# Performance work log

Hardware: AMD Instinct MI355X
Metric: run time of the kernel (lower is better)

## Reference

```python
import jax, jax.numpy as jnp
import numpy as np
from jax import lax

SLOPE = 0.1  # LeakyRelu(0.1)
DN = ('NCHW', 'OIHW', 'NCHW')


def _xavier(key, shape, cin, cout):
    bound = 2.0 / (cout + cin) ** 0.5
    return jax.random.uniform(key, shape, jnp.float32, -bound, bound)


def setup_inputs() -> dict:
    key = jax.random.key(0)
    ks = jax.random.split(key, 9)
    x = jax.random.normal(ks[0], (8, 3, 256, 256), jnp.float32)
    # Conv2d always adds bias in forward (even with bias=False flag), so biases included.
    w1 = _xavier(ks[1], (48, 3, 3, 3), 3, 48)
    b1 = _xavier(ks[2], (48,), 3, 48)
    w2 = _xavier(ks[3], (48, 48, 3, 3), 48, 48)
    b2 = _xavier(ks[4], (48,), 48, 48)
    w3 = _xavier(ks[5], (48, 48, 3, 3), 48, 48)
    b3 = _xavier(ks[6], (48,), 48, 48)
    w4 = _xavier(ks[7], (48, 48, 3, 3), 48, 48)
    b4 = _xavier(ks[8], (48,), 48, 48)
    return {"x": x, "w1": w1, "b1": b1, "w2": w2, "b2": b2,
            "w3": w3, "b3": b3, "w4": w4, "b4": b4}


def _convblock(x, w, b):
    # 3x3 stride-1 pad-1 conv (original does unfold + matmul; math identical)
    y = lax.conv_general_dilated(x, w, (1, 1), [(1, 1), (1, 1)], dimension_numbers=DN)
    y = y + b[None, :, None, None]
    # LeakyReLU: x * (mask*(1-s)+s) == where(x>0, x, s*x)
    return jnp.where(y > 0, y, SLOPE * y)


def _maxpool2(x):
    n, c, h, w = x.shape
    return x.reshape(n, c, h // 2, 2, w // 2, 2).max(axis=(3, 5))


def reference(x, w1, b1, w2, b2, w3, b3, w4, b4):
    # encoder01: conv(3->48) + conv(48->48) + maxpool
    h = _convblock(x, w1, b1)
    h = _convblock(h, w2, b2)
    h = _maxpool2(h)
    # encoder2: conv(48->48) + maxpool
    h = _convblock(h, w3, b3)
    h = _maxpool2(h)
    # encoder3: conv(48->48) + maxpool
    h = _convblock(h, w4, b4)
    h = _maxpool2(h)
    return h  # (8, 48, 32, 32)
```

## Files before the change

### kernel.cpp

```cpp
#include <hip/hip_runtime.h>
#include <hip/hip_bf16.h>

typedef _Float16 half_t;
typedef _Float16 f16x8 __attribute__((ext_vector_type(8)));
typedef _Float16 f16x4 __attribute__((ext_vector_type(4)));
typedef float f32x4 __attribute__((ext_vector_type(4)));

#define LEAKY 0.1f

__global__ __launch_bounds__(512) void prep_w_k(const float* __restrict__ w1,
                                                const float* __restrict__ w2,
                                                half_t* __restrict__ wp1,
                                                half_t* __restrict__ wp2)
{
    int t = blockIdx.x * 512 + threadIdx.x;
    if (t < 1920) {
        int co = t / 40, kk = t % 40;
        float v = 0.f;
        if (kk < 27) {
            int tap = kk / 3, ci = kk % 3;
            v = w1[((co * 3 + ci) * 3 + tap / 3) * 3 + tap % 3];
        }
        wp1[t] = (half_t)v;
        return;
    }
    int t2 = t - 1920;
    if (t2 >= 23040) return;
    int tap = t2 / 2304, r = t2 % 2304;
    int ci8 = r / 384, r2 = r % 384;
    int mm = r2 / 24, r3 = r2 % 24;
    int nt = r3 / 8, j = r3 % 8;
    int co = nt * 16 + mm, ci = ci8 * 8 + j;
    float v = 0.f;
    if (tap < 9) v = w2[((co * 48 + ci) * 3 + tap / 3) * 3 + tap % 3];
    wp2[t2] = (half_t)v;
}

__global__ __launch_bounds__(512, 4) void conv12_k(const float* __restrict__ x,
                                                   const half_t* __restrict__ wp1,
                                                   const float* __restrict__ b1,
                                                   const half_t* __restrict__ wp2,
                                                   const float* __restrict__ b2,
                                                   const float* __restrict__ w3,
                                                   const float* __restrict__ w4,
                                                   half_t* __restrict__ wp34,
                                                   half_t* __restrict__ out)
{
    __shared__ alignas(16) half_t in_t[624 * 56];
    __shared__ alignas(16) half_t xt[21][36][4];
    __shared__ alignas(16) half_t w1t[1920];

    const int tid = threadIdx.x;
    const int n = blockIdx.z;
    const int hblk = blockIdx.x * 16, wblk = blockIdx.y * 32;
    const int lane = tid & 63, hp = tid >> 6;
    const int m = lane & 15, g = lane >> 4;

    {
        int bid = blockIdx.x + 16 * (blockIdx.y + 8 * blockIdx.z);
        int t2 = bid * 512 + tid;
        if (t2 < 46080) {
            int layer = t2 / 23040, r0 = t2 % 23040;
            int tap = r0 / 2304, r = r0 % 2304;
            int ci8 = r / 384, r2 = r % 384;
            int mm = r2 / 24, r3 = r2 % 24;
            int nt = r3 / 8, j = r3 % 8;
            int co = nt * 16 + mm, ci = ci8 * 8 + j;
            const float* src = layer ? w4 : w3;
            float v = 0.f;
            if (tap < 9) v = src[((co * 48 + ci) * 3 + tap / 3) * 3 + tap % 3];
            wp34[t2] = (half_t)v;
        }
    }
    {
        const uint4* s = (const uint4*)wp1;
        uint4* d = (uint4*)w1t;
        if (tid < 240) d[tid] = s[tid];
    }
    for (int c = tid; c < 2268; c += 512) {
        int ci = c / 756, rem = c % 756;
        int row = rem / 36, col = rem % 36;
        int gh = hblk - 2 + row, gw = wblk - 2 + col;
        float v = 0.f;
        if ((unsigned)gh < 256u && (unsigned)gw < 256u)
            v = x[((n * 3 + ci) * 256 + gh) * 256 + gw];
        xt[row][col][ci] = (half_t)v;
    }
    __syncthreads();

    int xoff[8];
    #pragma unroll
    for (int j = 0; j < 8; ++j) {
        int k = g * 8 + j;
        int tap = k / 3, ci = k - 3 * tap;
        int dr = tap / 3, ds = tap - 3 * dr;
        xoff[j] = (k < 27) ? ((dr * 36 + ds) * 8 + ci * 2) : 0;
    }
    f16x8 wf[3];
    float bb1[12];
    #pragma unroll
    for (int nt = 0; nt < 3; ++nt) {
        wf[nt] = *(const f16x8*)((const char*)w1t + (nt * 16 + m) * 80 + g * 16);
        float4 bv = *(const float4*)(b1 + nt * 16 + 4 * g);
        bb1[nt * 4 + 0] = bv.x; bb1[nt * 4 + 1] = bv.y;
        bb1[nt * 4 + 2] = bv.z; bb1[nt * 4 + 3] = bv.w;
    }
    const char* xtb = (const char*)&xt[0][0][0];
    for (int t = hp; t < 39; t += 8) {
        int px = t * 16 + m;
        int row = px / 34, col = px - row * 34;
        int pxb = (row * 36 + col) * 8;
        f16x8 pf;
        #pragma unroll
        for (int j = 0; j < 8; ++j)
            pf[j] = *(const half_t*)(xtb + pxb + xoff[j]);
        bool inb = ((unsigned)(hblk - 1 + row) < 256u) && ((unsigned)(wblk - 1 + col) < 256u);
        #pragma unroll
        for (int nt = 0; nt < 3; ++nt) {
            f32x4 d = {0.f, 0.f, 0.f, 0.f};
            d = __builtin_amdgcn_mfma_f32_16x16x32_f16(wf[nt], pf, d, 0, 0, 0);
            f16x4 o;
            #pragma unroll
            for (int j = 0; j < 4; ++j) {
                float v = d[j] + bb1[nt * 4 + j];
                v = v > 0.f ? v : LEAKY * v;
                o[j] = inb ? (half_t)v : (half_t)0.f;
            }
            *(f16x4*)(&in_t[px * 56 + nt * 16 + 4 * g]) = o;
        }
    }

    const int hpar = m & 1, wloc = m >> 1;
    const int abase = hp * 7616;
    const char* ib = (const char*)in_t;
    const char* bp = (const char*)wp2 + m * 48;

    f16x8 bf[4][3], af[4];

#define BLOAD(S) { \
    int kc = 4 * (S) + g; int tap = kc / 6, ci8 = kc - tap * 6; \
    int boff = tap * 4608 + ci8 * 768; \
    bf[(S) & 3][0] = *(const f16x8*)(bp + boff); \
    bf[(S) & 3][1] = *(const f16x8*)(bp + boff + 16); \
    bf[(S) & 3][2] = *(const f16x8*)(bp + boff + 32); }
#define ALOAD(S) { \
    int kc = 4 * (S) + g; int tap = kc / 6, ci8 = kc - tap * 6; \
    int dr = tap / 3, ds = tap - 3 * dr; \
    if (tap == 9) { dr = 0; ds = 0; } \
    int aoff = ((hpar + dr) * 34 + (wloc + ds)) * 112 + ci8 * 16 + abase; \
    af[0] = *(const f16x8*)(ib + aoff); \
    af[1] = *(const f16x8*)(ib + aoff + 896); \
    af[2] = *(const f16x8*)(ib + aoff + 1792); \
    af[3] = *(const f16x8*)(ib + aoff + 2688); }
#define MM(P) { \
    __builtin_amdgcn_s_setprio(1); \
    _Pragma("unroll") \
    for (int mt = 0; mt < 4; ++mt) { \
        acc[mt][0] = __builtin_amdgcn_mfma_f32_16x16x32_f16(af[mt], bf[P][0], acc[mt][0], 0, 0, 0); \
        acc[mt][1] = __builtin_amdgcn_mfma_f32_16x16x32_f16(af[mt], bf[P][1], acc[mt][1], 0, 0, 0); \
        acc[mt][2] = __builtin_amdgcn_mfma_f32_16x16x32_f16(af[mt], bf[P][2], acc[mt][2], 0, 0, 0); \
    } \
    __builtin_amdgcn_s_setprio(0); }

    BLOAD(0); BLOAD(1); BLOAD(2); BLOAD(3);
    __syncthreads();

    f32x4 acc[4][3];
    #pragma unroll
    for (int mt = 0; mt < 4; ++mt)
        #pragma unroll
        for (int nt = 0; nt < 3; ++nt)
            acc[mt][nt] = (f32x4){0.f, 0.f, 0.f, 0.f};

    #pragma unroll
    for (int s = 0; s < 14; ++s) {
        ALOAD(s);
        MM(s & 3);
        if (s < 10) BLOAD(s + 4);
    }
#undef BLOAD
#undef ALOAD
#undef MM

    int hq = blockIdx.x * 8 + hp;
    #pragma unroll
    for (int nt = 0; nt < 3; ++nt) {
        int co = nt * 16 + m;
        float bb = b2[co];
        #pragma unroll
        for (int mt = 0; mt < 4; ++mt) {
            float pmax = -1e30f;
            #pragma unroll
            for (int j = 0; j < 4; ++j) {
                float v = acc[mt][nt][j] + bb;
                v = v > 0.f ? v : LEAKY * v;
                pmax = fmaxf(pmax, v);
            }
            int wq = blockIdx.y * 16 + mt * 4 + g;
            out[((n * 128 + hq) * 128 + wq) * 48 + co] = (half_t)pmax;
        }
    }
}

template<int H, int W, int MT, int NTS, bool FINAL>
__global__ __launch_bounds__(256, 4)
void convpool4_k(const half_t* __restrict__ in,
                 const half_t* __restrict__ wp,
                 const float* __restrict__ bias,
                 void* __restrict__ outv)
{
    constexpr int HO = H / 2, WO = W / 2;
    constexpr int TC = 8 * MT + 2;
    constexpr int NU4 = 10 * TC * 6;

    __shared__ alignas(16) half_t in_t[10][TC][56];

    int tid = threadIdx.x;
    int n = blockIdx.z & 7, ntb = blockIdx.z >> 3;
    int hblk = blockIdx.x * 8, wblk = blockIdx.y * (8 * MT);
    int lane = tid & 63, hp = tid >> 6;
    int m = lane & 15, g = lane >> 4;
    int hpar = m & 1, wloc = m >> 1;

    {
        const uint4* s4 = (const uint4*)in;
        uint4* d = (uint4*)&in_t[0][0][0];
        #pragma unroll
        for (int i = 0; i < (NU4 + 255) / 256; ++i) {
            int c = tid + i * 256;
            if (c < NU4) {
                int row = c / (TC * 6);
                int rem = c - row * (TC * 6);
                int pix = rem / 6;
                int sub = rem - pix * 6;
                int gh = hblk - 1 + row, gw = wblk - 1 + pix;
                uint4 v = {0u, 0u, 0u, 0u};
                if ((unsigned)gh < (unsigned)H && (unsigned)gw < (unsigned)W)
                    v = s4[((n * H + gh) * W + gw) * 6 + sub];
                d[(row * TC + pix) * 7 + sub] = v;
            }
        }
    }

    int abase = hp * 2 * TC * 112;
    const char* ib = (const char*)&in_t[0][0][0];
    const char* bp = (const char*)wp + m * 48 + ntb * NTS * 16;

    f16x8 bf[4][NTS], a[MT];

#define BLOAD(S) { \
    int kc = 4 * (S) + g; int tap = kc / 6, ci8 = kc - tap * 6; \
    int boff = tap * 4608 + ci8 * 768; \
    _Pragma("unroll") \
    for (int nt = 0; nt < NTS; ++nt) \
        bf[(S) & 3][nt] = *(const f16x8*)(bp + boff + nt * 16); }

    BLOAD(0); BLOAD(1); BLOAD(2); BLOAD(3);

    f32x4 acc[MT][NTS];
    #pragma unroll
    for (int mt = 0; mt < MT; ++mt)
        #pragma unroll
        for (int nt = 0; nt < NTS; ++nt)
            acc[mt][nt] = (f32x4){0.f, 0.f, 0.f, 0.f};

    __syncthreads();

    #pragma unroll
    for (int s = 0; s < 14; ++s) {
        int kc = 4 * s + g;
        int tap = kc / 6, ci8 = kc - tap * 6;
        int dr = tap / 3, ds = tap - 3 * dr;
        if (tap == 9) { dr = 0; ds = 0; }
        int aoff = ((hpar + dr) * TC + (wloc + ds)) * 112 + ci8 * 16;
        #pragma unroll
        for (int mt = 0; mt < MT; ++mt)
            a[mt] = *(const f16x8*)(ib + abase + aoff + mt * 896);
        __builtin_amdgcn_s_setprio(1);
        #pragma unroll
        for (int mt = 0; mt < MT; ++mt)
            #pragma unroll
            for (int nt = 0; nt < NTS; ++nt)
                acc[mt][nt] = __builtin_amdgcn_mfma_f32_16x16x32_f16(a[mt], bf[s & 3][nt], acc[mt][nt], 0, 0, 0);
        __builtin_amdgcn_s_setprio(0);
        if (s < 10) BLOAD(s + 4);
    }
#undef BLOAD

    int hq = blockIdx.x * 4 + hp;
    #pragma unroll
    for (int nt = 0; nt < NTS; ++nt) {
        int co = (ntb * NTS + nt) * 16 + m;
        float bb = bias[co];
        #pragma unroll
        for (int mt = 0; mt < MT; ++mt) {
            float pmax = -1e30f;
            #pragma unroll
            for (int j = 0; j < 4; ++j) {
                float v = acc[mt][nt][j] + bb;
                v = v > 0.f ? v : LEAKY * v;
                pmax = fmaxf(pmax, v);
            }
            int wq = blockIdx.y * (4 * MT) + mt * 4 + g;
            if (FINAL)
                ((float*)outv)[(((long)n * 48 + co) * HO + hq) * WO + wq] = pmax;
            else
                ((half_t*)outv)[((n * HO + hq) * WO + wq) * 48 + co] = (half_t)pmax;
        }
    }
}

extern "C" void kernel_launch(void* const* d_in, const int* in_sizes, int n_in,
                              void* d_out, int out_size, void* d_ws, size_t ws_size,
                              hipStream_t stream)
{
    const float* x  = (const float*)d_in[0];
    const float* w1 = (const float*)d_in[1];
    const float* b1 = (const float*)d_in[2];
    const float* w2 = (const float*)d_in[3];
    const float* b2 = (const float*)d_in[4];
    const float* w3 = (const float*)d_in[5];
    const float* b3 = (const float*)d_in[6];
    const float* w4 = (const float*)d_in[7];
    const float* b4 = (const float*)d_in[8];

    half_t* Wb = (half_t*)d_ws;
    half_t* wp1  = Wb;
    half_t* wp2  = Wb + 2048;
    half_t* wp34 = wp2 + 23040;
    half_t* act2 = wp34 + 46080;
    half_t* act3 = act2 + 6291456;

    prep_w_k<<<dim3(49), 512, 0, stream>>>(w1, w2, wp1, wp2);

    conv12_k<<<dim3(16, 8, 8), 512, 0, stream>>>(x, wp1, b1, wp2, b2, w3, w4, wp34, act2);
    convpool4_k<128, 128, 4, 3, false><<<dim3(16, 4, 8), 256, 0, stream>>>(act2, wp34, b3, act3);
    convpool4_k<64, 64, 2, 1, true><<<dim3(8, 4, 24), 256, 0, stream>>>(act3, wp34 + 23040, b4, d_out);
}
```

Baseline: 57.98 us.

## Fuse conv3 and conv4 stages into one kernel with halo recompute

Replaces the two separate convpool launches for layers 3 and 4 with a single conv34 kernel. Each block recomputes conv3+pool over a halo tile from act2, keeps the pooled result in shared memory and runs conv4+pool from it. Conv3 weights are held in registers with swapped MFMA operands. Weight repacking for w3/w4 moves from conv12 into the prep kernel. This removes the act3 round trip through global memory and one launch, at the cost of redundant halo computation, heavy register use (launch bounds 256,2) and only 512 blocks.

```diff
diff --git a/kernel.cpp b/kernel.cpp
--- a/kernel.cpp
+++ b/kernel.cpp
@@ -10,8 +10,12 @@
 
 __global__ __launch_bounds__(512) void prep_w_k(const float* __restrict__ w1,
                                                 const float* __restrict__ w2,
+                                                const float* __restrict__ w3,
+                                                const float* __restrict__ w4,
                                                 half_t* __restrict__ wp1,
-                                                half_t* __restrict__ wp2)
+                                                half_t* __restrict__ wp2,
+                                                half_t* __restrict__ wp3s,
+                                                half_t* __restrict__ wp4)
 {
     int t = blockIdx.x * 512 + threadIdx.x;
     if (t < 1920) {
@@ -24,16 +28,40 @@
         wp1[t] = (half_t)v;
         return;
     }
-    int t2 = t - 1920;
-    if (t2 >= 23040) return;
-    int tap = t2 / 2304, r = t2 % 2304;
-    int ci8 = r / 384, r2 = r % 384;
-    int mm = r2 / 24, r3 = r2 % 24;
-    int nt = r3 / 8, j = r3 % 8;
-    int co = nt * 16 + mm, ci = ci8 * 8 + j;
-    float v = 0.f;
-    if (tap < 9) v = w2[((co * 48 + ci) * 3 + tap / 3) * 3 + tap % 3];
-    wp2[t2] = (half_t)v;
+    t -= 1920;
+    if (t < 23040) {
+        int tap = t / 2304, r = t % 2304;
+        int ci8 = r / 384, r2 = r % 384;
+        int mm = r2 / 24, r3 = r2 % 24;
+        int nt = r3 / 8, j = r3 % 8;
+        int co = nt * 16 + mm, ci = ci8 * 8 + j;
+        float v = 0.f;
+        if (tap < 9) v = w2[((co * 48 + ci) * 3 + tap / 3) * 3 + tap % 3];
+        wp2[t] = (half_t)v;
+        return;
+    }
+    t -= 23040;
+    if (t < 21504) {
+        int co = t / 448, r = t % 448;
+        int kc = r / 8, j = r % 8;
+        int tap = kc / 6, ci8 = kc % 6;
+        int ci = ci8 * 8 + j;
+        float v = 0.f;
+        if (tap < 9) v = w3[((co * 48 + ci) * 3 + tap / 3) * 3 + tap % 3];
+        wp3s[t] = (half_t)v;
+        return;
+    }
+    t -= 21504;
+    if (t < 23040) {
+        int tap = t / 2304, r = t % 2304;
+        int ci8 = r / 384, r2 = r % 384;
+        int mm = r2 / 24, r3 = r2 % 24;
+        int nt = r3 / 8, j = r3 % 8;
+        int co = nt * 16 + mm, ci = ci8 * 8 + j;
+        float v = 0.f;
+        if (tap < 9) v = w4[((co * 48 + ci) * 3 + tap / 3) * 3 + tap % 3];
+        wp4[t] = (half_t)v;
+    }
 }
 
 __global__ __launch_bounds__(512, 4) void conv12_k(const float* __restrict__ x,
@@ -41,9 +69,6 @@
                                                    const float* __restrict__ b1,
                                                    const half_t* __restrict__ wp2,
                                                    const float* __restrict__ b2,
-                                                   const float* __restrict__ w3,
-                                                   const float* __restrict__ w4,
-                                                   half_t* __restrict__ wp34,
                                                    half_t* __restrict__ out)
 {
     __shared__ alignas(16) half_t in_t[624 * 56];
@@ -56,22 +81,6 @@
     const int lane = tid & 63, hp = tid >> 6;
     const int m = lane & 15, g = lane >> 4;
 
-    {
-        int bid = blockIdx.x + 16 * (blockIdx.y + 8 * blockIdx.z);
-        int t2 = bid * 512 + tid;
-        if (t2 < 46080) {
-            int layer = t2 / 23040, r0 = t2 % 23040;
-            int tap = r0 / 2304, r = r0 % 2304;
-            int ci8 = r / 384, r2 = r % 384;
-            int mm = r2 / 24, r3 = r2 % 24;
-            int nt = r3 / 8, j = r3 % 8;
-            int co = nt * 16 + mm, ci = ci8 * 8 + j;
-            const float* src = layer ? w4 : w3;
-            float v = 0.f;
-            if (tap < 9) v = src[((co * 48 + ci) * 3 + tap / 3) * 3 + tap % 3];
-            wp34[t2] = (half_t)v;
-        }
-    }
     {
         const uint4* s = (const uint4*)wp1;
         uint4* d = (uint4*)w1t;
@@ -202,111 +211,143 @@
     }
 }
 
-template<int H, int W, int MT, int NTS, bool FINAL>
-__global__ __launch_bounds__(256, 4)
-void convpool4_k(const half_t* __restrict__ in,
-                 const half_t* __restrict__ wp,
-                 const float* __restrict__ bias,
-                 void* __restrict__ outv)
+__global__ __launch_bounds__(256, 2) void conv34_k(const half_t* __restrict__ act2,
+                                                   const half_t* __restrict__ wp3s,
+                                                   const float* __restrict__ b3,
+                                                   const half_t* __restrict__ wp4,
+                                                   const float* __restrict__ b4,
+                                                   float* __restrict__ out)
 {
-    constexpr int HO = H / 2, WO = W / 2;
-    constexpr int TC = 8 * MT + 2;
-    constexpr int NU4 = 10 * TC * 6;
-
-    __shared__ alignas(16) half_t in_t[10][TC][56];
-
-    int tid = threadIdx.x;
-    int n = blockIdx.z & 7, ntb = blockIdx.z >> 3;
-    int hblk = blockIdx.x * 8, wblk = blockIdx.y * (8 * MT);
-    int lane = tid & 63, hp = tid >> 6;
-    int m = lane & 15, g = lane >> 4;
-    int hpar = m & 1, wloc = m >> 1;
+    __shared__ alignas(16) half_t a2t[22 * 22 * 56];
+    __shared__ alignas(16) half_t in_t[100 * 56];
+
+    const int tid = threadIdx.x;
+    const int n = blockIdx.z;
+    const int bx = blockIdx.x, by = blockIdx.y;
+    const int lane = tid & 63, hp = tid >> 6;
+    const int m = lane & 15, g = lane >> 4;
 
     {
-        const uint4* s4 = (const uint4*)in;
-        uint4* d = (uint4*)&in_t[0][0][0];
-        #pragma unroll
-        for (int i = 0; i < (NU4 + 255) / 256; ++i) {
+        const uint4* s4 = (const uint4*)act2;
+        uint4* d = (uint4*)a2t;
+        #pragma unroll
+        for (int i = 0; i < 14; ++i) {
             int c = tid + i * 256;
-            if (c < NU4) {
-                int row = c / (TC * 6);
-                int rem = c - row * (TC * 6);
-                int pix = rem / 6;
-                int sub = rem - pix * 6;
-                int gh = hblk - 1 + row, gw = wblk - 1 + pix;
+            if (c < 3388) {
+                int row = c / 132, rem = c - row * 132;
+                int col = rem / 6, sub = rem - col * 6;
+                int gh = bx * 16 - 3 + row, gw = by * 16 - 3 + col;
                 uint4 v = {0u, 0u, 0u, 0u};
-                if ((unsigned)gh < (unsigned)H && (unsigned)gw < (unsigned)W)
-                    v = s4[((n * H + gh) * W + gw) * 6 + sub];
-                d[(row * TC + pix) * 7 + sub] = v;
+                if ((unsigned)gh < 128u && (unsigned)gw < 128u)
+                    v = s4[((n * 128 + gh) * 128 + gw) * 6 + sub];
+                d[(row * 22 + col) * 7 + sub] = v;
             }
         }
     }
 
-    int abase = hp * 2 * TC * 112;
-    const char* ib = (const char*)&in_t[0][0][0];
-    const char* bp = (const char*)wp + m * 48 + ntb * NTS * 16;
-
-    f16x8 bf[4][NTS], a[MT];
-
-#define BLOAD(S) { \
-    int kc = 4 * (S) + g; int tap = kc / 6, ci8 = kc - tap * 6; \
-    int boff = tap * 4608 + ci8 * 768; \
-    _Pragma("unroll") \
-    for (int nt = 0; nt < NTS; ++nt) \
-        bf[(S) & 3][nt] = *(const f16x8*)(bp + boff + nt * 16); }
-
-    BLOAD(0); BLOAD(1); BLOAD(2); BLOAD(3);
-
-    f32x4 acc[MT][NTS];
-    #pragma unroll
-    for (int mt = 0; mt < MT; ++mt)
-        #pragma unroll
-        for (int nt = 0; nt < NTS; ++nt)
-            acc[mt][nt] = (f32x4){0.f, 0.f, 0.f, 0.f};
-
-    __syncthreads();
-
+    const char* w3p = (const char*)wp3s + m * 896;
+    f16x8 wf3[14][3];
+    #pragma unroll
+    for (int s = 0; s < 14; ++s) {
+        int kc = 4 * s + g;
+        #pragma unroll
+        for (int nt = 0; nt < 3; ++nt)
+            wf3[s][nt] = *(const f16x8*)(w3p + nt * 14336 + kc * 16);
+    }
+    int aoff3[14];
     #pragma unroll
     for (int s = 0; s < 14; ++s) {
         int kc = 4 * s + g;
         int tap = kc / 6, ci8 = kc - tap * 6;
         int dr = tap / 3, ds = tap - 3 * dr;
         if (tap == 9) { dr = 0; ds = 0; }
-        int aoff = ((hpar + dr) * TC + (wloc + ds)) * 112 + ci8 * 16;
-        #pragma unroll
-        for (int mt = 0; mt < MT; ++mt)
-            a[mt] = *(const f16x8*)(ib + abase + aoff + mt * 896);
-        __builtin_amdgcn_s_setprio(1);
-        #pragma unroll
-        for (int mt = 0; mt < MT; ++mt)
-            #pragma unroll
-            for (int nt = 0; nt < NTS; ++nt)
-                acc[mt][nt] = __builtin_amdgcn_mfma_f32_16x16x32_f16(a[mt], bf[s & 3][nt], acc[mt][nt], 0, 0, 0);
-        __builtin_amdgcn_s_setprio(0);
-        if (s < 10) BLOAD(s + 4);
-    }
-#undef BLOAD
-
-    int hq = blockIdx.x * 4 + hp;
-    #pragma unroll
-    for (int nt = 0; nt < NTS; ++nt) {
-        int co = (ntb * NTS + nt) * 16 + m;
-        float bb = bias[co];
-        #pragma unroll
-        for (int mt = 0; mt < MT; ++mt) {
-            float pmax = -1e30f;
+        aoff3[s] = (dr * 22 + ds) * 112 + ci8 * 16;
+    }
+    float bb3[12];
+    #pragma unroll
+    for (int nt = 0; nt < 3; ++nt) {
+        float4 bv = *(const float4*)(b3 + nt * 16 + 4 * g);
+        bb3[nt * 4 + 0] = bv.x; bb3[nt * 4 + 1] = bv.y;
+        bb3[nt * 4 + 2] = bv.z; bb3[nt * 4 + 3] = bv.w;
+    }
+    __syncthreads();
+
+    const char* ab = (const char*)a2t;
+    const int prow = m >> 2, pcol = m & 3;
+    for (int t = hp; t < 25; t += 4) {
+        int tr = t / 5, tc = t - tr * 5;
+        int rr = tr * 4 + prow, cc = tc * 4 + pcol;
+        int pxoff = (rr * 22 + cc) * 112;
+        f32x4 d3[3];
+        d3[0] = (f32x4){0.f, 0.f, 0.f, 0.f};
+        d3[1] = (f32x4){0.f, 0.f, 0.f, 0.f};
+        d3[2] = (f32x4){0.f, 0.f, 0.f, 0.f};
+        #pragma unroll
+        for (int s = 0; s < 14; ++s) {
+            f16x8 pa = *(const f16x8*)(ab + pxoff + aoff3[s]);
+            d3[0] = __builtin_amdgcn_mfma_f32_16x16x32_f16(wf3[s][0], pa, d3[0], 0, 0, 0);
+            d3[1] = __builtin_amdgcn_mfma_f32_16x16x32_f16(wf3[s][1], pa, d3[1], 0, 0, 0);
+            d3[2] = __builtin_amdgcn_mfma_f32_16x16x32_f16(wf3[s][2], pa, d3[2], 0, 0, 0);
+        }
+        int pp_r = tr * 2 + (m >> 3);
+        int pp_c = tc * 2 + ((m & 2) >> 1);
+        bool valid = ((unsigned)(bx * 8 - 1 + pp_r) < 64u) &&
+                     ((unsigned)(by * 8 - 1 + pp_c) < 64u);
+        #pragma unroll
+        for (int nt = 0; nt < 3; ++nt) {
+            f16x4 o;
             #pragma unroll
             for (int j = 0; j < 4; ++j) {
-                float v = acc[mt][nt][j] + bb;
-                v = v > 0.f ? v : LEAKY * v;
-                pmax = fmaxf(pmax, v);
+                float v = d3[nt][j];
+                v = fmaxf(v, __shfl_xor(v, 1));
+                v = fmaxf(v, __shfl_xor(v, 4));
+                float r = v + bb3[nt * 4 + j];
+                r = r > 0.f ? r : LEAKY * r;
+                o[j] = valid ? (half_t)r : (half_t)0.f;
             }
-            int wq = blockIdx.y * (4 * MT) + mt * 4 + g;
-            if (FINAL)
-                ((float*)outv)[(((long)n * 48 + co) * HO + hq) * WO + wq] = pmax;
-            else
-                ((half_t*)outv)[((n * HO + hq) * WO + wq) * 48 + co] = (half_t)pmax;
-        }
+            if ((m & 5) == 0)
+                *(f16x4*)(&in_t[(pp_r * 10 + pp_c) * 56 + nt * 16 + 4 * g]) = o;
+        }
+    }
+    __syncthreads();
+
+    const int hpar = m & 1, wloc = m >> 1;
+    const char* ib = (const char*)in_t;
+    const char* bp = (const char*)wp4 + m * 48;
+    const int abase = hp * 2240;
+
+    f32x4 acc[3];
+    #pragma unroll
+    for (int nt = 0; nt < 3; ++nt) acc[nt] = (f32x4){0.f, 0.f, 0.f, 0.f};
+
+    #pragma unroll
+    for (int s = 0; s < 14; ++s) {
+        int kc = 4 * s + g;
+        int tap = kc / 6, ci8 = kc - tap * 6;
+        int dr = tap / 3, ds = tap - 3 * dr;
+        if (tap == 9) { dr = 0; ds = 0; }
+        int aoff = ((hpar + dr) * 10 + (wloc + ds)) * 112 + ci8 * 16 + abase;
+        int boff = tap * 4608 + ci8 * 768;
+        f16x8 a = *(const f16x8*)(ib + aoff);
+        acc[0] = __builtin_amdgcn_mfma_f32_16x16x32_f16(a, *(const f16x8*)(bp + boff), acc[0], 0, 0, 0);
+        acc[1] = __builtin_amdgcn_mfma_f32_16x16x32_f16(a, *(const f16x8*)(bp + boff + 16), acc[1], 0, 0, 0);
+        acc[2] = __builtin_amdgcn_mfma_f32_16x16x32_f16(a, *(const f16x8*)(bp + boff + 32), acc[2], 0, 0, 0);
+    }
+
+    int hq = bx * 4 + hp;
+    int wq = by * 4 + g;
+    #pragma unroll
+    for (int nt = 0; nt < 3; ++nt) {
+        int co = nt * 16 + m;
+        float bb = b4[co];
+        float pmax = -1e30f;
+        #pragma unroll
+        for (int j = 0; j < 4; ++j) {
+            float v = acc[nt][j] + bb;
+            v = v > 0.f ? v : LEAKY * v;
+            pmax = fmaxf(pmax, v);
+        }
+        out[(((long)n * 48 + co) * 32 + hq) * 32 + wq] = pmax;
     }
 }
 
@@ -327,13 +368,12 @@
     half_t* Wb = (half_t*)d_ws;
     half_t* wp1  = Wb;
     half_t* wp2  = Wb + 2048;
-    half_t* wp34 = wp2 + 23040;
-    half_t* act2 = wp34 + 46080;
-    half_t* act3 = act2 + 6291456;
-
-    prep_w_k<<<dim3(49), 512, 0, stream>>>(w1, w2, wp1, wp2);
-
-    conv12_k<<<dim3(16, 8, 8), 512, 0, stream>>>(x, wp1, b1, wp2, b2, w3, w4, wp34, act2);
-    convpool4_k<128, 128, 4, 3, false><<<dim3(16, 4, 8), 256, 0, stream>>>(act2, wp34, b3, act3);
-    convpool4_k<64, 64, 2, 1, true><<<dim3(8, 4, 24), 256, 0, stream>>>(act3, wp34 + 23040, b4, d_out);
+    half_t* wp3s = wp2 + 23040;
+    half_t* wp4  = wp3s + 21504;
+    half_t* act2 = wp4 + 23040;
+
+    prep_w_k<<<dim3(136), 512, 0, stream>>>(w1, w2, w3, w4, wp1, wp2, wp3s, wp4);
+
+    conv12_k<<<dim3(16, 8, 8), 512, 0, stream>>>(x, wp1, b1, wp2, b2, act2);
+    conv34_k<<<dim3(8, 8, 8), 256, 0, stream>>>(act2, wp3s, b3, wp4, b4, (float*)d_out);
 }
```

After: 67.17 us. 15.8% more time.

## Store padded activations and read conv A operands directly from global memory

Applied to the files above, without the earlier changes.

Intermediate activations are now written into zero-bordered padded buffers, and the borders are zeroed in the prep kernel along with all weight repacking for layers 2-4. The later conv+pool kernels drop the shared-memory staging and the syncthreads, and load MFMA A fragments straight from global memory (through cache) using precomputed offsets. The B-operand prefetch depth shrinks from 4 to 2. This removes the LDS fill and bounds checks, at the cost of relying on L1/L2 for reuse of overlapping input rows and of longer load latency on the A operand.

```diff
diff --git a/kernel.cpp b/kernel.cpp
--- a/kernel.cpp
+++ b/kernel.cpp
@@ -10,8 +10,12 @@
 
 __global__ __launch_bounds__(512) void prep_w_k(const float* __restrict__ w1,
                                                 const float* __restrict__ w2,
+                                                const float* __restrict__ w3,
+                                                const float* __restrict__ w4,
                                                 half_t* __restrict__ wp1,
-                                                half_t* __restrict__ wp2)
+                                                half_t* __restrict__ wp234,
+                                                half_t* __restrict__ act2p,
+                                                half_t* __restrict__ act3p)
 {
     int t = blockIdx.x * 512 + threadIdx.x;
     if (t < 1920) {
@@ -24,16 +28,44 @@
         wp1[t] = (half_t)v;
         return;
     }
-    int t2 = t - 1920;
-    if (t2 >= 23040) return;
-    int tap = t2 / 2304, r = t2 % 2304;
-    int ci8 = r / 384, r2 = r % 384;
-    int mm = r2 / 24, r3 = r2 % 24;
-    int nt = r3 / 8, j = r3 % 8;
-    int co = nt * 16 + mm, ci = ci8 * 8 + j;
-    float v = 0.f;
-    if (tap < 9) v = w2[((co * 48 + ci) * 3 + tap / 3) * 3 + tap % 3];
-    wp2[t2] = (half_t)v;
+    t -= 1920;
+    if (t < 3 * 23040) {
+        int layer = t / 23040, r0 = t % 23040;
+        int tap = r0 / 2304, r = r0 % 2304;
+        int ci8 = r / 384, r2 = r % 384;
+        int mm = r2 / 24, r3 = r2 % 24;
+        int nt = r3 / 8, j = r3 % 8;
+        int co = nt * 16 + mm, ci = ci8 * 8 + j;
+        const float* src = layer == 0 ? w2 : (layer == 1 ? w3 : w4);
+        float v = 0.f;
+        if (tap < 9) v = src[((co * 48 + ci) * 3 + tap / 3) * 3 + tap % 3];
+        wp234[t] = (half_t)v;
+        return;
+    }
+    t -= 3 * 23040;
+    const uint4 z = {0u, 0u, 0u, 0u};
+    if (t < 8 * 516 * 6) {
+        int sub = t % 6, r = t / 6;
+        int b = r % 516, n = r / 516;
+        int row, col;
+        if (b < 130)      { row = 0;   col = b; }
+        else if (b < 260) { row = 129; col = b - 130; }
+        else if (b < 388) { row = b - 260 + 1; col = 0; }
+        else              { row = b - 388 + 1; col = 129; }
+        ((uint4*)act2p)[((n * 130 + row) * 130 + col) * 6 + sub] = z;
+        return;
+    }
+    t -= 8 * 516 * 6;
+    if (t < 8 * 260 * 6) {
+        int sub = t % 6, r = t / 6;
+        int b = r % 260, n = r / 260;
+        int row, col;
+        if (b < 66)       { row = 0;  col = b; }
+        else if (b < 132) { row = 65; col = b - 66; }
+        else if (b < 196) { row = b - 132 + 1; col = 0; }
+        else              { row = b - 196 + 1; col = 65; }
+        ((uint4*)act3p)[((n * 66 + row) * 66 + col) * 6 + sub] = z;
+    }
 }
 
 __global__ __launch_bounds__(512, 4) void conv12_k(const float* __restrict__ x,
@@ -41,9 +73,6 @@
                                                    const float* __restrict__ b1,
                                                    const half_t* __restrict__ wp2,
                                                    const float* __restrict__ b2,
-                                                   const float* __restrict__ w3,
-                                                   const float* __restrict__ w4,
-                                                   half_t* __restrict__ wp34,
                                                    half_t* __restrict__ out)
 {
     __shared__ alignas(16) half_t in_t[624 * 56];
@@ -56,22 +85,6 @@
     const int lane = tid & 63, hp = tid >> 6;
     const int m = lane & 15, g = lane >> 4;
 
-    {
-        int bid = blockIdx.x + 16 * (blockIdx.y + 8 * blockIdx.z);
-        int t2 = bid * 512 + tid;
-        if (t2 < 46080) {
-            int layer = t2 / 23040, r0 = t2 % 23040;
-            int tap = r0 / 2304, r = r0 % 2304;
-            int ci8 = r / 384, r2 = r % 384;
-            int mm = r2 / 24, r3 = r2 % 24;
-            int nt = r3 / 8, j = r3 % 8;
-            int co = nt * 16 + mm, ci = ci8 * 8 + j;
-            const float* src = layer ? w4 : w3;
-            float v = 0.f;
-            if (tap < 9) v = src[((co * 48 + ci) * 3 + tap / 3) * 3 + tap % 3];
-            wp34[t2] = (half_t)v;
-        }
-    }
     {
         const uint4* s = (const uint4*)wp1;
         uint4* d = (uint4*)w1t;
@@ -197,93 +210,74 @@
                 pmax = fmaxf(pmax, v);
             }
             int wq = blockIdx.y * 16 + mt * 4 + g;
-            out[((n * 128 + hq) * 128 + wq) * 48 + co] = (half_t)pmax;
+            out[((n * 130 + hq + 1) * 130 + (wq + 1)) * 48 + co] = (half_t)pmax;
         }
     }
 }
 
 template<int H, int W, int MT, int NTS, bool FINAL>
 __global__ __launch_bounds__(256, 4)
-void convpool4_k(const half_t* __restrict__ in,
-                 const half_t* __restrict__ wp,
-                 const float* __restrict__ bias,
-                 void* __restrict__ outv)
+void convpool_d_k(const half_t* __restrict__ in,
+                  const half_t* __restrict__ wp,
+                  const float* __restrict__ bias,
+                  void* __restrict__ outv)
 {
     constexpr int HO = H / 2, WO = W / 2;
-    constexpr int TC = 8 * MT + 2;
-    constexpr int NU4 = 10 * TC * 6;
-
-    __shared__ alignas(16) half_t in_t[10][TC][56];
-
-    int tid = threadIdx.x;
-    int n = blockIdx.z & 7, ntb = blockIdx.z >> 3;
-    int hblk = blockIdx.x * 8, wblk = blockIdx.y * (8 * MT);
-    int lane = tid & 63, hp = tid >> 6;
-    int m = lane & 15, g = lane >> 4;
-    int hpar = m & 1, wloc = m >> 1;
-
-    {
-        const uint4* s4 = (const uint4*)in;
-        uint4* d = (uint4*)&in_t[0][0][0];
-        #pragma unroll
-        for (int i = 0; i < (NU4 + 255) / 256; ++i) {
-            int c = tid + i * 256;
-            if (c < NU4) {
-                int row = c / (TC * 6);
-                int rem = c - row * (TC * 6);
-                int pix = rem / 6;
-                int sub = rem - pix * 6;
-                int gh = hblk - 1 + row, gw = wblk - 1 + pix;
-                uint4 v = {0u, 0u, 0u, 0u};
-                if ((unsigned)gh < (unsigned)H && (unsigned)gw < (unsigned)W)
-                    v = s4[((n * H + gh) * W + gw) * 6 + sub];
-                d[(row * TC + pix) * 7 + sub] = v;
-            }
-        }
-    }
-
-    int abase = hp * 2 * TC * 112;
-    const char* ib = (const char*)&in_t[0][0][0];
-    const char* bp = (const char*)wp + m * 48 + ntb * NTS * 16;
-
-    f16x8 bf[4][NTS], a[MT];
-
-#define BLOAD(S) { \
-    int kc = 4 * (S) + g; int tap = kc / 6, ci8 = kc - tap * 6; \
-    int boff = tap * 4608 + ci8 * 768; \
-    _Pragma("unroll") \
-    for (int nt = 0; nt < NTS; ++nt) \
-        bf[(S) & 3][nt] = *(const f16x8*)(bp + boff + nt * 16); }
-
-    BLOAD(0); BLOAD(1); BLOAD(2); BLOAD(3);
-
-    f32x4 acc[MT][NTS];
-    #pragma unroll
-    for (int mt = 0; mt < MT; ++mt)
-        #pragma unroll
-        for (int nt = 0; nt < NTS; ++nt)
-            acc[mt][nt] = (f32x4){0.f, 0.f, 0.f, 0.f};
-
-    __syncthreads();
-
+    constexpr int WP = W + 2;
+    constexpr int ROWB = WP * 96;
+
+    const int tid = threadIdx.x;
+    const int n = blockIdx.z & 7, ntb = blockIdx.z >> 3;
+    const int hblk = blockIdx.x * 8, wblk = blockIdx.y * (8 * MT);
+    const int lane = tid & 63, hp = tid >> 6;
+    const int m = lane & 15, g = lane >> 4;
+    const int hpar = m & 1, wloc = m >> 1;
+
+    const char* ap = (const char*)in
+        + ((long)(n * (H + 2) + hblk + 2 * hp) * WP) * 96;
+    int aoff[14];
     #pragma unroll
     for (int s = 0; s < 14; ++s) {
         int kc = 4 * s + g;
         int tap = kc / 6, ci8 = kc - tap * 6;
         int dr = tap / 3, ds = tap - 3 * dr;
         if (tap == 9) { dr = 0; ds = 0; }
-        int aoff = ((hpar + dr) * TC + (wloc + ds)) * 112 + ci8 * 16;
+        aoff[s] = (hpar + dr) * ROWB + (wloc + ds) * 96 + ci8 * 16;
+    }
+    const int acol = wblk * 96;
+    const char* bp = (const char*)wp + m * 48 + ntb * NTS * 16;
+
+    f16x8 bf[2][NTS], a[MT];
+
+#define BLOAD(S, P) { \
+    int kc = 4 * (S) + g; int tap = kc / 6, ci8 = kc - tap * 6; \
+    int boff = tap * 4608 + ci8 * 768; \
+    _Pragma("unroll") \
+    for (int nt = 0; nt < NTS; ++nt) \
+        bf[P][nt] = *(const f16x8*)(bp + boff + nt * 16); }
+
+    BLOAD(0, 0); BLOAD(1, 1);
+
+    f32x4 acc[MT][NTS];
+    #pragma unroll
+    for (int mt = 0; mt < MT; ++mt)
+        #pragma unroll
+        for (int nt = 0; nt < NTS; ++nt)
+            acc[mt][nt] = (f32x4){0.f, 0.f, 0.f, 0.f};
+
+    #pragma unroll
+    for (int s = 0; s < 14; ++s) {
         #pragma unroll
         for (int mt = 0; mt < MT; ++mt)
-            a[mt] = *(const f16x8*)(ib + abase + aoff + mt * 896);
+            a[mt] = *(const f16x8*)(ap + acol + aoff[s] + mt * 768);
         __builtin_amdgcn_s_setprio(1);
         #pragma unroll
         for (int mt = 0; mt < MT; ++mt)
             #pragma unroll
             for (int nt = 0; nt < NTS; ++nt)
-                acc[mt][nt] = __builtin_amdgcn_mfma_f32_16x16x32_f16(a[mt], bf[s & 3][nt], acc[mt][nt], 0, 0, 0);
+                acc[mt][nt] = __builtin_amdgcn_mfma_f32_16x16x32_f16(a[mt], bf[s & 1][nt], acc[mt][nt], 0, 0, 0);
         __builtin_amdgcn_s_setprio(0);
-        if (s < 10) BLOAD(s + 4);
+        if (s < 12) BLOAD(s + 2, s & 1);
     }
 #undef BLOAD
 
@@ -305,7 +299,7 @@
             if (FINAL)
                 ((float*)outv)[(((long)n * 48 + co) * HO + hq) * WO + wq] = pmax;
             else
-                ((half_t*)outv)[((n * HO + hq) * WO + wq) * 48 + co] = (half_t)pmax;
+                ((half_t*)outv)[((n * (HO + 2) + hq + 1) * (WO + 2) + wq + 1) * 48 + co] = (half_t)pmax;
         }
     }
 }
@@ -325,15 +319,16 @@
     const float* b4 = (const float*)d_in[8];
 
     half_t* Wb = (half_t*)d_ws;
-    half_t* wp1  = Wb;
-    half_t* wp2  = Wb + 2048;
-    half_t* wp34 = wp2 + 23040;
-    half_t* act2 = wp34 + 46080;
-    half_t* act3 = act2 + 6291456;
-
-    prep_w_k<<<dim3(49), 512, 0, stream>>>(w1, w2, wp1, wp2);
-
-    conv12_k<<<dim3(16, 8, 8), 512, 0, stream>>>(x, wp1, b1, wp2, b2, w3, w4, wp34, act2);
-    convpool4_k<128, 128, 4, 3, false><<<dim3(16, 4, 8), 256, 0, stream>>>(act2, wp34, b3, act3);
-    convpool4_k<64, 64, 2, 1, true><<<dim3(8, 4, 24), 256, 0, stream>>>(act3, wp34 + 23040, b4, d_out);
+    half_t* wp1   = Wb;
+    half_t* wp2   = Wb + 2048;
+    half_t* wp3   = wp2 + 23040;
+    half_t* wp4   = wp3 + 23040;
+    half_t* act2p = wp4 + 23040;
+    half_t* act3p = act2p + 6489600;
+
+    prep_w_k<<<dim3(212), 512, 0, stream>>>(w1, w2, w3, w4, wp1, wp2, act2p, act3p);
+
+    conv12_k<<<dim3(16, 8, 8), 512, 0, stream>>>(x, wp1, b1, wp2, b2, act2p);
+    convpool_d_k<128, 128, 4, 3, false><<<dim3(16, 4, 8), 256, 0, stream>>>(act2p, wp3, b3, act3p);
+    convpool_d_k<64, 64, 2, 1, true><<<dim3(8, 4, 24), 256, 0, stream>>>(act3p, wp4, b4, d_out);
 }
```

New measurement: 61.61 us. 1.06x slower.
